# Kernel optimization log

Measured on AMD Instinct MI355X. Metric: run time of the kernel, lower is better.

## Reference

```python
import jax, jax.numpy as jnp
import numpy as np

DIM = 1024
SRC_DIM = 1152
NUM_HEADS = 16
HEAD_DIM = DIM // NUM_HEADS  # 64
ROPE_BASE = 10000.0


def rope_tables(seq_len, head_dim):
    # matches RotaryPositionEmbedding: inv_freq over even indices, emb = cat([freqs, freqs])
    inv_freq = 1.0 / (ROPE_BASE ** (jnp.arange(0, head_dim, 2, dtype=jnp.float32) / head_dim))
    t = jnp.arange(seq_len, dtype=jnp.float32)
    freqs = t[:, None] * inv_freq[None, :]          # (L, D/2)
    emb = jnp.concatenate([freqs, freqs], axis=-1)  # (L, D)
    return jnp.cos(emb), jnp.sin(emb)


def rotate_half(x):
    # interleaved rotation as in the torch code
    x1 = x[..., ::2]
    x2 = x[..., 1::2]
    return jnp.stack((-x2, x1), axis=-1).reshape(x.shape)


def apply_rope(t, cos, sin):
    # t: (B, H, L, D); cos/sin: (L, D)
    return t * cos[None, None] + rotate_half(t) * sin[None, None]


def setup_inputs() -> dict:
    key = jax.random.key(0)
    ks = jax.random.split(key, 10)
    B, T, K = 2, 2048, 2048
    s_q = 1.0 / np.sqrt(DIM)
    s_kv = 1.0 / np.sqrt(SRC_DIM)
    return {
        "x": jax.random.normal(ks[0], (B, T, DIM), jnp.float32),
        "context": jax.random.normal(ks[1], (B, K, SRC_DIM), jnp.float32),
        "Wq": jax.random.normal(ks[2], (DIM, DIM), jnp.float32) * s_q,
        "bq": jnp.zeros((DIM,), jnp.float32),
        "Wk": jax.random.normal(ks[3], (DIM, SRC_DIM), jnp.float32) * s_kv,
        "bk": jnp.zeros((DIM,), jnp.float32),
        "Wv": jax.random.normal(ks[4], (DIM, SRC_DIM), jnp.float32) * s_kv,
        "bv": jnp.zeros((DIM,), jnp.float32),
        "Wo": jax.random.normal(ks[5], (DIM, DIM), jnp.float32) * s_q,
        "bo": jnp.zeros((DIM,), jnp.float32),
    }


def reference(x, context, Wq, bq, Wk, bk, Wv, bv, Wo, bo):
    B, T, C = x.shape
    K = context.shape[1]
    H, D = NUM_HEADS, HEAD_DIM

    q = x @ Wq.T + bq                 # (B, T, C)
    k = context @ Wk.T + bk           # (B, K, C)
    v = context @ Wv.T + bv           # (B, K, C)

    q = q.reshape(B, T, H, D).transpose(0, 2, 1, 3)  # (B, H, T, D)
    k = k.reshape(B, K, H, D).transpose(0, 2, 1, 3)  # (B, H, K, D)
    v = v.reshape(B, K, H, D).transpose(0, 2, 1, 3)

    cos_q, sin_q = rope_tables(T, D)
    cos_k, sin_k = rope_tables(K, D)
    q = apply_rope(q, cos_q, sin_q)
    k = apply_rope(k, cos_k, sin_k)

    scale = 1.0 / np.sqrt(D).astype(np.float32)
    scores = jnp.einsum('bhtd,bhkd->bhtk', q, k) * scale  # (B, H, T, K)
    weights = jax.nn.softmax(scores, axis=-1)
    out = jnp.einsum('bhtk,bhkd->bhtd', weights, v)        # (B, H, T, D)
    out = out.transpose(0, 2, 1, 3).reshape(B, T, C)
    return out @ Wo.T + bo
```

## Files before the change

kernel.cpp:

```cpp
#include <hip/hip_runtime.h>
#include <hip/hip_bf16.h>
#include <stdint.h>

typedef unsigned short u16;
typedef __attribute__((ext_vector_type(8))) short bf16x8;
typedef __attribute__((ext_vector_type(8))) unsigned short u16x8;
typedef __attribute__((ext_vector_type(4))) float f32x4;

#define BM 128
#define BN 128
#define BK 32
#define QBK 64
#define QSCALE 0.18033688f

__device__ __forceinline__ u16 f2bf(float f) {
    union { float f; uint32_t u; } v; v.f = f;
    uint32_t r = v.u + 0x7FFFu + ((v.u >> 16) & 1u);
    return (u16)(r >> 16);
}

__device__ __forceinline__ uint32_t cvt_pk_bf16(float lo, float hi) {
    uint32_t r;
    asm("v_cvt_pk_bf16_f32 %0, %1, %2" : "=v"(r) : "v"(lo), "v"(hi));
    return r;
}

__device__ __forceinline__ float fexp2(float x) {
    float r;
    asm volatile("v_exp_f32 %0, %1\n\ts_nop 0" : "=v"(r) : "v"(x));
    return r;
}

__device__ __forceinline__ void gload_lds16(const void* g, void* l) {
    __builtin_amdgcn_global_load_lds(
        (const __attribute__((address_space(1))) void*)(g),
        (__attribute__((address_space(3))) void*)(l),
        16, 0, 0);
}

__global__ void prep_kernel(const float* __restrict__ x, const float* __restrict__ ctx,
                            const float* __restrict__ Wq, const float* __restrict__ Wk,
                            const float* __restrict__ Wv, const float* __restrict__ Wo,
                            u16* __restrict__ xb, u16* __restrict__ cb,
                            u16* __restrict__ wqb, u16* __restrict__ wkb,
                            u16* __restrict__ wvb, u16* __restrict__ wob,
                            float2* __restrict__ cs) {
    int t = blockIdx.x * 256 + threadIdx.x;
    if (t < 3342336) {
        const float* src; u16* dst; int base;
        if      (t < 1048576) { src = x;   dst = xb;  base = 0; }
        else if (t < 2228224) { src = ctx; dst = cb;  base = 1048576; }
        else if (t < 2490368) { src = Wq;  dst = wqb; base = 2228224; }
        else if (t < 2785280) { src = Wk;  dst = wkb; base = 2490368; }
        else if (t < 3080192) { src = Wv;  dst = wvb; base = 2785280; }
        else                  { src = Wo;  dst = wob; base = 3080192; }
        int i = (t - base) * 4;
        float4 v = *reinterpret_cast<const float4*>(src + i);
        ushort4 o = { f2bf(v.x), f2bf(v.y), f2bf(v.z), f2bf(v.w) };
        *reinterpret_cast<ushort4*>(dst + i) = o;
    } else {
        int idx = t - 3342336;
        int tt = idx >> 5, j = idx & 31;
        float invf = 1.0f / powf(10000.0f, (float)(2 * j) / 64.0f);
        float ang = (float)tt * invf;
        cs[idx] = make_float2(cosf(ang), sinf(ang));
    }
}

__global__ __launch_bounds__(256, 3)
void qkv_gemm(const u16* __restrict__ xb, const u16* __restrict__ cb,
              const u16* __restrict__ wqb, const u16* __restrict__ wkb,
              const u16* __restrict__ wvb,
              const float* __restrict__ bq, const float* __restrict__ bk,
              const float* __restrict__ bv,
              u16* __restrict__ qo, u16* __restrict__ ko, u16* __restrict__ vo,
              const float2* __restrict__ cs)
{
    __shared__ __align__(16) u16 As[BM * QBK];
    __shared__ __align__(16) u16 Bs[BN * QBK];
    const int bid = blockIdx.x;
    const int wg = (bid & 7) * 96 + (bid >> 3);
    const int seg = wg >> 8, inner = wg & 255;
    const u16* A; const u16* Bm; const float* bias; u16* C;
    int N, K, mbase, nbase, rope, brow;
    float oscale;
    if (seg == 0)      { A = xb;  Bm = wqb; bias = bq; C = qo; N = 1024; K = 1024; rope = 1; brow = 0; oscale = QSCALE; nbase = (inner & 7) * BN;  mbase = (inner >> 3) * BM; }
    else if (seg == 1) { A = cb;  Bm = wkb; bias = bk; C = ko; N = 1024; K = 1152; rope = 1; brow = 0; oscale = 1.0f;   nbase = (inner & 7) * BN;  mbase = (inner >> 3) * BM; }
    else               { A = wvb; Bm = cb;  bias = bv; C = vo; N = 4096; K = 1152; rope = 0; brow = 1; oscale = 1.0f;   nbase = (inner & 31) * BN; mbase = (inner >> 5) * BM; }

    const int tid = threadIdx.x;
    const int wid = tid >> 6, lane = tid & 63;
    const int wr = wid >> 1, wc = wid & 1;
    const int l15 = lane & 15, l4 = lane >> 4;
    const int r8 = lane >> 3;
    const int cp = lane & 7;
    const int cl = cp ^ r8;

    f32x4 acc[4][4];
#pragma unroll
    for (int i = 0; i < 4; i++)
#pragma unroll
        for (int j = 0; j < 4; j++) acc[i][j] = (f32x4){0.f, 0.f, 0.f, 0.f};

    for (int k0 = 0; k0 < K; k0 += QBK) {
#pragma unroll
        for (int q = 0; q < 4; ++q) {
            int sg = wid * 4 + q;
            int row = sg * 8 + r8;
            gload_lds16(A  + (size_t)(mbase + row) * K + k0 + cl * 8, (void*)(As + sg * 512));
            gload_lds16(Bm + (size_t)(nbase + row) * K + k0 + cl * 8, (void*)(Bs + sg * 512));
        }
        __syncthreads();
        bf16x8 af[2][4], bfv[2][4];
#pragma unroll
        for (int kk = 0; kk < 2; kk++) {
#pragma unroll
            for (int i = 0; i < 4; i++) {
                int r = wr * 64 + i * 16 + l15;
                af[kk][i] = *(const bf16x8*)(As + r * 64 + (((kk * 4 + l4) ^ (r & 7)) * 8));
            }
#pragma unroll
            for (int j = 0; j < 4; j++) {
                int r = wc * 64 + j * 16 + l15;
                bfv[kk][j] = *(const bf16x8*)(Bs + r * 64 + (((kk * 4 + l4) ^ (r & 7)) * 8));
            }
        }
        __builtin_amdgcn_s_setprio(1);
#pragma unroll
        for (int kk = 0; kk < 2; kk++)
#pragma unroll
            for (int i = 0; i < 4; i++)
#pragma unroll
                for (int j = 0; j < 4; j++)
                    acc[i][j] = __builtin_amdgcn_mfma_f32_16x16x32_bf16(af[kk][i], bfv[kk][j], acc[i][j], 0, 0, 0);
        __builtin_amdgcn_s_setprio(0);
        __syncthreads();
    }

#pragma unroll
    for (int i = 0; i < 4; i++) {
#pragma unroll
        for (int j = 0; j < 4; j++) {
#pragma unroll
            for (int r = 0; r < 4; r++) {
                int row = mbase + wr * 64 + i * 16 + l4 * 4 + r;
                int col = nbase + wc * 64 + j * 16 + l15;
                float v = acc[i][j][r] + (brow ? bias[row] : bias[col]);
                if (rope) {
                    float part = __shfl_xor(v, 1);
                    float2 c2 = cs[(row & 2047) * 32 + (col & 31)];
                    v = v * c2.x + ((col & 1) ? part * c2.y : -part * c2.y);
                    v *= oscale;
                }
                C[(size_t)row * N + col] = f2bf(v);
            }
        }
    }
}

__global__ __launch_bounds__(256, 2)
void gemm_out(const u16* __restrict__ A, const u16* __restrict__ B,
              const float* __restrict__ bias, float* __restrict__ C,
              int M, int N, int K)
{
    __shared__ __align__(16) u16 As[2][BM * BK];
    __shared__ __align__(16) u16 Bs[2][64 * BK];
    const int tid = threadIdx.x;
    const int wid = tid >> 6, lane = tid & 63;
    const int wr = wid >> 1, wc = wid & 1;
    const int l15 = lane & 15, l4 = lane >> 4;
    const int mbase = blockIdx.y * BM, nbase = blockIdx.x * 64;
    const int srow = lane >> 2;
    const int scol = (lane & 3) * 8;
    const int nk = K >> 5;

    f32x4 acc[4][2];
#pragma unroll
    for (int i = 0; i < 4; i++)
#pragma unroll
        for (int j = 0; j < 2; j++) acc[i][j] = (f32x4){0.f, 0.f, 0.f, 0.f};

    auto stage = [&](int bs, int k0) {
#pragma unroll
        for (int q = 0; q < 2; ++q) {
            int seg = wid * 2 + q;
            int row = seg * 16 + srow;
            gload_lds16(A + (size_t)(mbase + row) * K + k0 + scol, (void*)(&As[bs][seg * 512]));
        }
        {
            int row = wid * 16 + srow;
            gload_lds16(B + (size_t)(nbase + row) * K + k0 + scol, (void*)(&Bs[bs][wid * 512]));
        }
    };

    stage(0, 0);
    __syncthreads();
    int buf = 0;
    for (int ks = 0; ks < nk; ++ks) {
        if (ks + 1 < nk) stage(buf ^ 1, (ks + 1) * BK);
        bf16x8 af[4], bfv[2];
#pragma unroll
        for (int i = 0; i < 4; i++)
            af[i] = *(const bf16x8*)(&As[buf][(wr * 64 + i * 16 + l15) * BK + l4 * 8]);
#pragma unroll
        for (int j = 0; j < 2; j++)
            bfv[j] = *(const bf16x8*)(&Bs[buf][(wc * 32 + j * 16 + l15) * BK + l4 * 8]);
#pragma unroll
        for (int i = 0; i < 4; i++)
#pragma unroll
            for (int j = 0; j < 2; j++)
                acc[i][j] = __builtin_amdgcn_mfma_f32_16x16x32_bf16(af[i], bfv[j], acc[i][j], 0, 0, 0);
        __syncthreads();
        buf ^= 1;
    }

#pragma unroll
    for (int i = 0; i < 4; i++)
#pragma unroll
        for (int j = 0; j < 2; j++)
#pragma unroll
            for (int r = 0; r < 4; r++) {
                int row = mbase + wr * 64 + i * 16 + l4 * 4 + r;
                int col = nbase + wc * 32 + j * 16 + l15;
                C[(size_t)row * N + col] = acc[i][j][r] + bias[col];
            }
}

__device__ __forceinline__ int invrow(int R) {
    return 32 * (R >> 5) + 8 * ((R >> 2) & 3) + 4 * ((R >> 4) & 1) + (R & 3);
}

__global__ __launch_bounds__(256, 4)
void attn_kernel(const u16* __restrict__ Qb, const u16* __restrict__ Kb,
                 const u16* __restrict__ VT, u16* __restrict__ Ob)
{
    const int qt = blockIdx.x;
    const int bh = blockIdx.y;
    const int b = bh >> 4, h = bh & 15;
    __shared__ __align__(16) u16 Ks[2][4096];
    __shared__ __align__(16) u16 Vs[2][4096];
    const int tid = threadIdx.x, wv = tid >> 6, lane = tid & 63;
    const int l15 = lane & 15, l4 = lane >> 4;

    const int r8 = lane >> 3;
    const int cp = lane & 7;
    const int cl = cp ^ r8;
    const int L0 = 2 * wv, L1 = 2 * wv + 1;
    const int RK0 = L0 * 8 + r8, RK1 = L1 * 8 + r8;
    const u16* ksrc0 = Kb + (size_t)(b * 2048 + invrow(RK0)) * 1024 + h * 64 + cl * 8;
    const u16* ksrc1 = Kb + (size_t)(b * 2048 + invrow(RK1)) * 1024 + h * 64 + cl * 8;
    const u16* vsrc0 = VT + (size_t)(h * 64 + RK0) * 4096 + b * 2048 + cl * 8;
    const u16* vsrc1 = VT + (size_t)(h * 64 + RK1) * 4096 + b * 2048 + cl * 8;

    const u16* qrow = Qb + (size_t)(b * 2048 + qt * 64 + wv * 16 + l15) * 1024 + h * 64;
    bf16x8 qf0 = *(const bf16x8*)(qrow + l4 * 8);
    bf16x8 qf1 = *(const bf16x8*)(qrow + 32 + l4 * 8);

    const int swz = l15 & 7;
    const int q0o = (l4 ^ swz) * 8;
    const int q1o = ((4 + l4) ^ swz) * 8;

    f32x4 accO[4];
    float denom = 0.f;
#pragma unroll
    for (int i = 0; i < 4; i++) accO[i] = (f32x4){0.f, 0.f, 0.f, 0.f};

    auto stage = [&](int bs, int kt) {
        gload_lds16(ksrc0 + (size_t)kt * 65536, (void*)&Ks[bs][L0 * 512]);
        gload_lds16(ksrc1 + (size_t)kt * 65536, (void*)&Ks[bs][L1 * 512]);
        gload_lds16(vsrc0 + kt * 64,            (void*)&Vs[bs][L0 * 512]);
        gload_lds16(vsrc1 + kt * 64,            (void*)&Vs[bs][L1 * 512]);
    };

    stage(0, 0);
    __syncthreads();

    int buf = 0;
    for (int kt = 0; kt < 32; ++kt) {
        if (kt < 31) stage(buf ^ 1, kt + 1);

        f32x4 s[4];
#pragma unroll
        for (int j = 0; j < 4; j++) s[j] = (f32x4){0.f, 0.f, 0.f, 0.f};
        __builtin_amdgcn_s_setprio(1);
#pragma unroll
        for (int j = 0; j < 4; j++) {
            const u16* rp = &Ks[buf][(j * 16 + l15) * 64];
            bf16x8 a0 = *(const bf16x8*)(rp + q0o);
            bf16x8 a1 = *(const bf16x8*)(rp + q1o);
            s[j] = __builtin_amdgcn_mfma_f32_16x16x32_bf16(a0, qf0, s[j], 0, 0, 0);
            s[j] = __builtin_amdgcn_mfma_f32_16x16x32_bf16(a1, qf1, s[j], 0, 0, 0);
        }
        __builtin_amdgcn_s_setprio(0);

        float p[4][4];
        float rs = 0.f;
#pragma unroll
        for (int j = 0; j < 4; j++)
#pragma unroll
            for (int r = 0; r < 4; r++) {
                p[j][r] = fexp2(s[j][r]);
                rs += p[j][r];
            }
        rs += __shfl_xor(rs, 16);
        rs += __shfl_xor(rs, 32);
        denom += rs;

        union { uint32_t u[4]; bf16x8 v; } B0u, B1u;
        B0u.u[0] = cvt_pk_bf16(p[0][0], p[0][1]);
        B0u.u[1] = cvt_pk_bf16(p[0][2], p[0][3]);
        B0u.u[2] = cvt_pk_bf16(p[1][0], p[1][1]);
        B0u.u[3] = cvt_pk_bf16(p[1][2], p[1][3]);
        B1u.u[0] = cvt_pk_bf16(p[2][0], p[2][1]);
        B1u.u[1] = cvt_pk_bf16(p[2][2], p[2][3]);
        B1u.u[2] = cvt_pk_bf16(p[3][0], p[3][1]);
        B1u.u[3] = cvt_pk_bf16(p[3][2], p[3][3]);

        __builtin_amdgcn_s_setprio(1);
#pragma unroll
        for (int i = 0; i < 4; i++) {
            const u16* vp = &Vs[buf][(i * 16 + l15) * 64];
            bf16x8 v0 = *(const bf16x8*)(vp + q0o);
            bf16x8 v1 = *(const bf16x8*)(vp + q1o);
            accO[i] = __builtin_amdgcn_mfma_f32_16x16x32_bf16(v0, B0u.v, accO[i], 0, 0, 0);
            accO[i] = __builtin_amdgcn_mfma_f32_16x16x32_bf16(v1, B1u.v, accO[i], 0, 0, 0);
        }
        __builtin_amdgcn_s_setprio(0);
        __syncthreads();
        buf ^= 1;
    }

    float rd = 1.0f / denom;
    u16* orow = Ob + (size_t)(b * 2048 + qt * 64 + wv * 16 + l15) * 1024 + h * 64;
#pragma unroll
    for (int i = 0; i < 4; i++) {
        uint2 st;
        st.x = cvt_pk_bf16(accO[i][0] * rd, accO[i][1] * rd);
        st.y = cvt_pk_bf16(accO[i][2] * rd, accO[i][3] * rd);
        *(uint2*)(orow + i * 16 + l4 * 4) = st;
    }
}

extern "C" void kernel_launch(void* const* d_in, const int* in_sizes, int n_in,
                              void* d_out, int out_size, void* d_ws, size_t ws_size,
                              hipStream_t stream) {
    const float* x   = (const float*)d_in[0];
    const float* ctx = (const float*)d_in[1];
    const float* Wq  = (const float*)d_in[2];
    const float* bq  = (const float*)d_in[3];
    const float* Wk  = (const float*)d_in[4];
    const float* bk  = (const float*)d_in[5];
    const float* Wv  = (const float*)d_in[6];
    const float* bv  = (const float*)d_in[7];
    const float* Wo  = (const float*)d_in[8];
    const float* bo  = (const float*)d_in[9];
    float* out = (float*)d_out;

    char* ws = (char*)d_ws;
    size_t off = 0;
    auto alloc = [&](size_t bytes) { void* p = ws + off; off += (bytes + 255) & ~255ULL; return p; };
    u16* x_bf  = (u16*)alloc(4096ULL * 1024 * 2);
    u16* c_bf  = (u16*)alloc(4096ULL * 1152 * 2);
    u16* wq_bf = (u16*)alloc(1024ULL * 1024 * 2);
    u16* wk_bf = (u16*)alloc(1024ULL * 1152 * 2);
    u16* wv_bf = (u16*)alloc(1024ULL * 1152 * 2);
    u16* wo_bf = (u16*)alloc(1024ULL * 1024 * 2);
    float2* cs = (float2*)alloc(2048ULL * 32 * 8);
    u16* q_bf  = (u16*)alloc(4096ULL * 1024 * 2);
    u16* k_bf  = (u16*)alloc(4096ULL * 1024 * 2);
    u16* vT    = (u16*)alloc(1024ULL * 4096 * 2);
    u16* a_bf  = (u16*)alloc(4096ULL * 1024 * 2);

    prep_kernel<<<13312, 256, 0, stream>>>(x, ctx, Wq, Wk, Wv, Wo,
                                           x_bf, c_bf, wq_bf, wk_bf, wv_bf, wo_bf, cs);
    qkv_gemm<<<768, 256, 0, stream>>>(x_bf, c_bf, wq_bf, wk_bf, wv_bf,
                                      bq, bk, bv, q_bf, k_bf, vT, cs);
    attn_kernel<<<dim3(32, 32), 256, 0, stream>>>(q_bf, k_bf, vT, a_bf);
    gemm_out<<<dim3(16, 32), 256, 0, stream>>>(a_bf, wo_bf, bo, out, 4096, 1024, 1024);
}
```

Measured before the change: 139.9 us.

## Load V fragments directly from global and skew PV one tile behind QK

The attention kernel drops the shared-memory V buffer. Each wave now loads its V fragments straight from global memory into registers. The loop is restructured so the QK^T MFMAs for tile kt run alongside the softmax and PV MFMAs for tile kt-1, using two alternating score register sets, with a final epilogue for the last tile. The aims are to halve LDS use and staging traffic and to hide exp/convert latency behind matrix work. The cost is that every wave re-reads the full V tile from global/L2 with only partly coalesced 16-byte loads, and register pressure goes up.

```diff
diff --git a/kernel.cpp b/kernel.cpp
--- a/kernel.cpp
+++ b/kernel.cpp
@@ -238,7 +238,6 @@
     const int bh = blockIdx.y;
     const int b = bh >> 4, h = bh & 15;
     __shared__ __align__(16) u16 Ks[2][4096];
-    __shared__ __align__(16) u16 Vs[2][4096];
     const int tid = threadIdx.x, wv = tid >> 6, lane = tid & 63;
     const int l15 = lane & 15, l4 = lane >> 4;
 
@@ -249,8 +248,8 @@
     const int RK0 = L0 * 8 + r8, RK1 = L1 * 8 + r8;
     const u16* ksrc0 = Kb + (size_t)(b * 2048 + invrow(RK0)) * 1024 + h * 64 + cl * 8;
     const u16* ksrc1 = Kb + (size_t)(b * 2048 + invrow(RK1)) * 1024 + h * 64 + cl * 8;
-    const u16* vsrc0 = VT + (size_t)(h * 64 + RK0) * 4096 + b * 2048 + cl * 8;
-    const u16* vsrc1 = VT + (size_t)(h * 64 + RK1) * 4096 + b * 2048 + cl * 8;
+
+    const u16* vrow0 = VT + (size_t)(h * 64 + l15) * 4096 + b * 2048 + l4 * 8;
 
     const u16* qrow = Qb + (size_t)(b * 2048 + qt * 64 + wv * 16 + l15) * 1024 + h * 64;
     bf16x8 qf0 = *(const bf16x8*)(qrow + l4 * 8);
@@ -265,47 +264,30 @@
 #pragma unroll
     for (int i = 0; i < 4; i++) accO[i] = (f32x4){0.f, 0.f, 0.f, 0.f};
 
-    auto stage = [&](int bs, int kt) {
+    auto stageK = [&](int bs, int kt) {
         gload_lds16(ksrc0 + (size_t)kt * 65536, (void*)&Ks[bs][L0 * 512]);
         gload_lds16(ksrc1 + (size_t)kt * 65536, (void*)&Ks[bs][L1 * 512]);
-        gload_lds16(vsrc0 + kt * 64,            (void*)&Vs[bs][L0 * 512]);
-        gload_lds16(vsrc1 + kt * 64,            (void*)&Vs[bs][L1 * 512]);
     };
 
-    stage(0, 0);
+    stageK(0, 0);
     __syncthreads();
 
-    int buf = 0;
-    for (int kt = 0; kt < 32; ++kt) {
-        if (kt < 31) stage(buf ^ 1, kt + 1);
-
-        f32x4 s[4];
-#pragma unroll
-        for (int j = 0; j < 4; j++) s[j] = (f32x4){0.f, 0.f, 0.f, 0.f};
-        __builtin_amdgcn_s_setprio(1);
-#pragma unroll
-        for (int j = 0; j < 4; j++) {
-            const u16* rp = &Ks[buf][(j * 16 + l15) * 64];
-            bf16x8 a0 = *(const bf16x8*)(rp + q0o);
-            bf16x8 a1 = *(const bf16x8*)(rp + q1o);
-            s[j] = __builtin_amdgcn_mfma_f32_16x16x32_bf16(a0, qf0, s[j], 0, 0, 0);
-            s[j] = __builtin_amdgcn_mfma_f32_16x16x32_bf16(a1, qf1, s[j], 0, 0, 0);
-        }
-        __builtin_amdgcn_s_setprio(0);
-
+    f32x4 sA[4], sB[4];
+    bf16x8 vf[4][2];
+
+    auto finish_tile = [&](f32x4 (&sold)[4]) {
         float p[4][4];
         float rs = 0.f;
 #pragma unroll
         for (int j = 0; j < 4; j++)
 #pragma unroll
             for (int r = 0; r < 4; r++) {
-                p[j][r] = fexp2(s[j][r]);
+                p[j][r] = fexp2(sold[j][r]);
                 rs += p[j][r];
             }
         rs += __shfl_xor(rs, 16);
         rs += __shfl_xor(rs, 32);
         denom += rs;
-
         union { uint32_t u[4]; bf16x8 v; } B0u, B1u;
         B0u.u[0] = cvt_pk_bf16(p[0][0], p[0][1]);
         B0u.u[1] = cvt_pk_bf16(p[0][2], p[0][3]);
@@ -315,19 +297,54 @@
         B1u.u[1] = cvt_pk_bf16(p[2][2], p[2][3]);
         B1u.u[2] = cvt_pk_bf16(p[3][0], p[3][1]);
         B1u.u[3] = cvt_pk_bf16(p[3][2], p[3][3]);
-
         __builtin_amdgcn_s_setprio(1);
 #pragma unroll
         for (int i = 0; i < 4; i++) {
-            const u16* vp = &Vs[buf][(i * 16 + l15) * 64];
-            bf16x8 v0 = *(const bf16x8*)(vp + q0o);
-            bf16x8 v1 = *(const bf16x8*)(vp + q1o);
-            accO[i] = __builtin_amdgcn_mfma_f32_16x16x32_bf16(v0, B0u.v, accO[i], 0, 0, 0);
-            accO[i] = __builtin_amdgcn_mfma_f32_16x16x32_bf16(v1, B1u.v, accO[i], 0, 0, 0);
+            accO[i] = __builtin_amdgcn_mfma_f32_16x16x32_bf16(vf[i][0], B0u.v, accO[i], 0, 0, 0);
+            accO[i] = __builtin_amdgcn_mfma_f32_16x16x32_bf16(vf[i][1], B1u.v, accO[i], 0, 0, 0);
         }
         __builtin_amdgcn_s_setprio(0);
+    };
+
+    auto body = [&](int kt, f32x4 (&snew)[4], f32x4 (&sold)[4]) {
+        if (kt > 0) {
+            const u16* vp = vrow0 + (size_t)(kt - 1) * 64;
+#pragma unroll
+            for (int i = 0; i < 4; i++) {
+                vf[i][0] = *(const bf16x8*)(vp + (size_t)i * 16 * 4096);
+                vf[i][1] = *(const bf16x8*)(vp + (size_t)i * 16 * 4096 + 32);
+            }
+        }
+#pragma unroll
+        for (int j = 0; j < 4; j++) snew[j] = (f32x4){0.f, 0.f, 0.f, 0.f};
+        const int kb = kt & 1;
+        __builtin_amdgcn_s_setprio(1);
+#pragma unroll
+        for (int j = 0; j < 4; j++) {
+            const u16* rp = &Ks[kb][(j * 16 + l15) * 64];
+            bf16x8 a0 = *(const bf16x8*)(rp + q0o);
+            bf16x8 a1 = *(const bf16x8*)(rp + q1o);
+            snew[j] = __builtin_amdgcn_mfma_f32_16x16x32_bf16(a0, qf0, snew[j], 0, 0, 0);
+            snew[j] = __builtin_amdgcn_mfma_f32_16x16x32_bf16(a1, qf1, snew[j], 0, 0, 0);
+        }
+        __builtin_amdgcn_s_setprio(0);
+        if (kt < 31) stageK(kb ^ 1, kt + 1);
+        if (kt > 0) finish_tile(sold);
         __syncthreads();
-        buf ^= 1;
+    };
+
+    for (int kt2 = 0; kt2 < 32; kt2 += 2) {
+        body(kt2, sA, sB);
+        body(kt2 + 1, sB, sA);
+    }
+    {
+        const u16* vp = vrow0 + (size_t)31 * 64;
+#pragma unroll
+        for (int i = 0; i < 4; i++) {
+            vf[i][0] = *(const bf16x8*)(vp + (size_t)i * 16 * 4096);
+            vf[i][1] = *(const bf16x8*)(vp + (size_t)i * 16 * 4096 + 32);
+        }
+        finish_tile(sB);
     }
 
     float rd = 1.0f / denom;
```

Result: slower. 218.7 us (+56.3%).
